# Kernel tuning notes

Measured on AMD Instinct MI355X. Metric: run time of the kernel, lower is better.

## Reference

```python
import jax, jax.numpy as jnp
import numpy as np

N = 50000      # nodes
E = 800000     # edges (avg degree 16)
DIN = 500      # input_dim
HID = 100      # hid_dim (fixed in module)
DOUT = 64      # output_dim
EPS = 1e-5     # LayerNorm eps (torch default)


def _layer_norm(x, g, b):
    mu = jnp.mean(x, axis=-1, keepdims=True)
    var = jnp.var(x, axis=-1, keepdims=True)
    return (x - mu) / jnp.sqrt(var + EPS) * g + b


def _gcn_conv(x, src, tgt, W, b):
    # PyG GCNConv: self-loops + symmetric normalization + linear + scatter-add
    h = x @ W  # [N, out]
    idx = jnp.arange(N)
    src_sl = jnp.concatenate([src, idx])
    tgt_sl = jnp.concatenate([tgt, idx])
    deg = jax.ops.segment_sum(jnp.ones(src_sl.shape, h.dtype), tgt_sl, num_segments=N)
    dinv = jnp.where(deg > 0, deg ** -0.5, 0.0)
    norm = dinv[src_sl] * dinv[tgt_sl]  # [E+N]
    out = jax.ops.segment_sum(h[src_sl] * norm[:, None], tgt_sl, num_segments=N)
    return out + b


def setup_inputs() -> dict:
    key = jax.random.key(0)
    ks = jax.random.split(key, 10)
    glorot = lambda k, fi, fo: jax.random.normal(k, (fi, fo), jnp.float32) * np.float32(1.0 / np.sqrt(fi))
    z = lambda d: jnp.zeros((d,), jnp.float32)
    return dict(
        data_x=jax.random.normal(ks[0], (N, DIN), jnp.float32),
        data_edge_index=jax.random.randint(ks[1], (2, E), 0, N),
        data_edge_attr=jnp.zeros((E,), jnp.int32),  # single relation type
        t_W1=glorot(ks[2], DIN, HID), t_b1=z(HID), t_g1=jnp.ones((HID,), jnp.float32), t_be1=z(HID),
        t_W2=glorot(ks[3], HID, HID), t_b2=z(HID), t_g2=jnp.ones((HID,), jnp.float32), t_be2=z(HID),
        r_Wrel=glorot(ks[4], HID, HID)[None],  # [n_relations=1, H, H]
        r_Wself=glorot(ks[5], HID, HID), r_b=z(HID),
        c1_W=glorot(ks[6], HID, HID), c1_b=z(HID),
        c2_W=glorot(ks[7], HID, DOUT), c2_b=z(DOUT),
    )


def reference(data_x, data_edge_index, data_edge_attr,
              t_W1, t_b1, t_g1, t_be1, t_W2, t_b2, t_g2, t_be2,
              r_Wrel, r_Wself, r_b, c1_W, c1_b, c2_W, c2_b):
    src, tgt = data_edge_index[0], data_edge_index[1]
    # transform: Linear -> LN -> ReLU -> Linear -> LN -> ReLU
    x = jax.nn.relu(_layer_norm(data_x @ t_W1 + t_b1, t_g1, t_be1))
    x = jax.nn.relu(_layer_norm(x @ t_W2 + t_b2, t_g2, t_be2))
    # RGCN, n_relations=1, n_layers=1: per-relation message + self transform
    msgs = x[src] @ r_Wrel[0]  # edge_attr is all relation 0
    x = x @ r_Wself + jax.ops.segment_sum(msgs, tgt, num_segments=N) + r_b
    x = jax.nn.relu(x)  # dropout = identity (eval)
    x = jax.nn.relu(_gcn_conv(x, src, tgt, c1_W, c1_b))
    x = _gcn_conv(x, src, tgt, c2_W, c2_b)
    return jax.nn.log_softmax(x, axis=1)
```

## Files before the change

### kernel.cpp

```cpp
#include <hip/hip_runtime.h>
#include <hip/hip_bf16.h>

typedef __attribute__((ext_vector_type(8))) short short8;
typedef __attribute__((ext_vector_type(8))) unsigned short ushort8;
typedef __attribute__((ext_vector_type(4))) float f32x4;

static constexpr int NN = 50000;
static constexpr int NE = 800000;
static constexpr int SCAN_B = 196;
static constexpr int NBLK = (NN + 63) / 64;

#define MFMA16x16x32 __builtin_amdgcn_mfma_f32_16x16x32_bf16

__device__ __forceinline__ float b2f(unsigned short u){
  unsigned v = ((unsigned)u) << 16;
  return __builtin_bit_cast(float, v);
}
__device__ __forceinline__ unsigned short f2b(float f){
  unsigned x = __builtin_bit_cast(unsigned, f);
  unsigned r = (x + 0x7fffu + ((x >> 16) & 1u)) >> 16;
  return (unsigned short)r;
}
__device__ __forceinline__ short8 u2s(ushort8 v){
  return __builtin_bit_cast(short8, v);
}

__device__ __align__(256) int   g_isf32;
__device__ __align__(256) unsigned short g_W1t  [112 * 512 + 512];
__device__ __align__(256) unsigned short g_W2t  [112 * 128];
__device__ __align__(256) unsigned short g_WselfT[112 * 128];
__device__ __align__(256) unsigned short g_WrelT [112 * 128];
__device__ __align__(256) unsigned short g_c1Wt [112 * 128];
__device__ __align__(256) unsigned short g_c2Wt [64 * 128];
__device__ __align__(256) unsigned short g_bufA[(size_t)NN * 128];
__device__ __align__(256) unsigned short g_bufB[(size_t)NN * 128];
__device__ __align__(256) unsigned short g_bufC[(size_t)NN * 128];
__device__ __align__(256) int   g_deg[NN];
__device__ __align__(256) int   g_rowptr[NN + 1];
__device__ __align__(256) int   g_colidx[NE];
__device__ __align__(256) int   g_epos[NE];
__device__ __align__(256) float g_dinv[NN];
__device__ __align__(256) int   g_partial[256];

__device__ __forceinline__ float ld_in(const void* p, int idx, int isf32){
  if (isf32) return ((const float*)p)[idx];
  return b2f(((const unsigned short*)p)[idx]);
}

__global__ void k_detect_zero(const unsigned short* __restrict__ x){
  if (blockIdx.x == 0){
    __shared__ int sh[256];
    int tid = threadIdx.x;
    int cnt = 0;
    for (int j = 0; j < 16; j++){
      unsigned short h = x[(size_t)(tid * 16 + j) * 2];
      int e = (h >> 7) & 0xFF;
      if (e >= 90 && e <= 160) cnt++;
    }
    sh[tid] = cnt;
    __syncthreads();
    for (int off = 128; off > 0; off >>= 1){
      if (tid < off) sh[tid] += sh[tid + off];
      __syncthreads();
    }
    if (tid == 0) g_isf32 = (sh[0] < 2458) ? 1 : 0;
  } else {
    int i = (blockIdx.x - 1) * 256 + threadIdx.x;
    if (i < NN) g_deg[i] = 0;
  }
}

__device__ __forceinline__ void xp_one(const void* W, unsigned short* Wt, int idx,
                                       int K, int Nc, int Kpad, int Npad, int isf32){
  int n = idx / Kpad;
  int k = idx - n * Kpad;
  float v = 0.f;
  if (n < Nc && k < K) v = ld_in(W, k * Nc + n, isf32);
  Wt[(k >> 5) * (Npad * 32) + n * 32 + (k & 31)] = f2b(v);
}
__global__ void k_transpose_all(const void* W1, const void* W2, const void* Wself,
                                const void* Wrel, const void* c1W, const void* c2W){
  int idx = blockIdx.x * 256 + threadIdx.x;
  const int isf32 = g_isf32;
  if (idx < 57344){ xp_one(W1, g_W1t, idx, 500, 100, 512, 112, isf32); return; }
  idx -= 57344;
  if (idx < 14336){ xp_one(W2,    g_W2t,    idx, 100, 100, 128, 112, isf32); return; }
  idx -= 14336;
  if (idx < 14336){ xp_one(Wself, g_WselfT, idx, 100, 100, 128, 112, isf32); return; }
  idx -= 14336;
  if (idx < 14336){ xp_one(Wrel,  g_WrelT,  idx, 100, 100, 128, 112, isf32); return; }
  idx -= 14336;
  if (idx < 14336){ xp_one(c1W,   g_c1Wt,   idx, 100, 100, 128, 112, isf32); return; }
  idx -= 14336;
  if (idx < 8192){  xp_one(c2W,   g_c2Wt,   idx, 100, 64,  128, 64, isf32); }
}

__global__ void k_deg(const int* __restrict__ tgt){
  int e = blockIdx.x * 256 + threadIdx.x;
  if (e < NE) g_epos[e] = atomicAdd(&g_deg[tgt[e]], 1);
}
__global__ __launch_bounds__(256) void k_scan1(){
  __shared__ int sh[256];
  int t = threadIdx.x;
  int i = blockIdx.x * 256 + t;
  int val = (i < NN) ? g_deg[i] : 0;
  sh[t] = val; __syncthreads();
#pragma unroll
  for (int off = 1; off < 256; off <<= 1){
    int v = (t >= off) ? sh[t - off] : 0;
    __syncthreads(); sh[t] += v; __syncthreads();
  }
  if (i < NN){ g_rowptr[i] = sh[t] - val; g_dinv[i] = rsqrtf((float)(val + 1)); }
  if (t == 255) g_partial[blockIdx.x] = sh[255];
}
__global__ __launch_bounds__(256) void k_scan2(){
  __shared__ int sh[256];
  int t = threadIdx.x;
  int val = (t < SCAN_B) ? g_partial[t] : 0;
  sh[t] = val; __syncthreads();
#pragma unroll
  for (int off = 1; off < 256; off <<= 1){
    int v = (t >= off) ? sh[t - off] : 0;
    __syncthreads(); sh[t] += v; __syncthreads();
  }
  if (t < SCAN_B) g_partial[t] = sh[t] - val;
  if (t == 255) g_rowptr[NN] = sh[255];
}
__global__ __launch_bounds__(256) void k_scan3(){
  int i = blockIdx.x * 256 + threadIdx.x;
  if (i < NN) g_rowptr[i] += g_partial[blockIdx.x];
}
__global__ void k_fill(const int* __restrict__ src, const int* __restrict__ tgt){
  int e = blockIdx.x * 256 + threadIdx.x;
  if (e >= NE) return;
  g_colidx[g_rowptr[tgt[e]] + g_epos[e]] = src[e];
}


template<int DO_LN>
__device__ __forceinline__ void wave_epi(const f32x4* acc, unsigned short* dst,
    int rstride, int grow0, int lane, int isf32,
    const void* bias, const void* gm, const void* be){
  const int m = lane & 15;
  const int q = lane >> 4;
  float bf_[7], gf_[7], ef_[7];
#pragma unroll
  for (int t = 0; t < 7; t++){
    int col = t * 16 + m;
    bool ok = col < 100;
    bf_[t] = ok ? ld_in(bias, col, isf32) : 0.f;
    if (DO_LN){
      gf_[t] = ok ? ld_in(gm, col, isf32) : 0.f;
      ef_[t] = ok ? ld_in(be, col, isf32) : 0.f;
    }
  }
#pragma unroll
  for (int r = 0; r < 4; r++){
    int rl = q * 4 + r;
    float vals[7], s1 = 0.f, s2 = 0.f;
#pragma unroll
    for (int t = 0; t < 7; t++){
      int col = t * 16 + m;
      float v = (col < 100) ? (acc[t][r] + bf_[t]) : 0.f;
      vals[t] = v; s1 += v; s2 += v * v;
    }
    if (DO_LN){
#pragma unroll
      for (int msk = 1; msk < 16; msk <<= 1){
        s1 += __shfl_xor(s1, msk, 64);
        s2 += __shfl_xor(s2, msk, 64);
      }
      float mu = s1 * 0.01f;
      float var = fmaxf(s2 * 0.01f - mu * mu, 0.f);
      float rstd = rsqrtf(var + 1e-5f);
#pragma unroll
      for (int t = 0; t < 7; t++)
        vals[t] = (vals[t] - mu) * rstd * gf_[t] + ef_[t];
    }
    if (grow0 + rl < NN){
      unsigned short* orow = dst + (size_t)rl * rstride;
#pragma unroll
      for (int t = 0; t < 7; t++){
        int col = t * 16 + m;
        float y = fmaxf(vals[t], 0.f);
        orow[col] = f2b((col < 100) ? y : 0.f);
      }
      orow[112 + m] = 0;
    }
  }
}

template<int MODE>
__device__ __forceinline__ void agg_tile(const unsigned short* __restrict__ x,
    unsigned short* aggT, int tid, int brow0){
  const int nl = tid >> 2;
  const int c0 = (tid & 3) * 32;
  const int node = min(brow0 + nl, NN - 1);
  const float wt = (MODE != 0) ? g_dinv[node] : 1.f;
  float a[32];
#pragma unroll
  for (int k = 0; k < 32; k++) a[k] = 0.f;
  const int p0 = g_rowptr[node], p1 = g_rowptr[node + 1];
  for (int p = p0; p < p1; p += 4){
    int s[4]; float wj[4];
#pragma unroll
    for (int j = 0; j < 4; j++){
      bool ok = (p + j) < p1;
      s[j] = ok ? g_colidx[p + j] : node;
      wj[j] = ok ? ((MODE != 0) ? g_dinv[s[j]] * wt : 1.f) : 0.f;
    }
    ushort8 r[4][4];
#pragma unroll
    for (int j = 0; j < 4; j++)
#pragma unroll
      for (int u = 0; u < 4; u++)
        r[j][u] = *reinterpret_cast<const ushort8*>(&x[(size_t)s[j] * 128 + c0 + u * 8]);
#pragma unroll
    for (int j = 0; j < 4; j++)
#pragma unroll
      for (int u = 0; u < 4; u++)
#pragma unroll
        for (int k = 0; k < 8; k++)
          a[u * 8 + k] += wj[j] * b2f((unsigned short)r[j][u][k]);
  }
  if (MODE != 0){
    float ws = wt * wt;
#pragma unroll
    for (int u = 0; u < 4; u++){
      ushort8 sv = *reinterpret_cast<const ushort8*>(&x[(size_t)node * 128 + c0 + u * 8]);
#pragma unroll
      for (int k = 0; k < 8; k++) a[u * 8 + k] += ws * b2f((unsigned short)sv[k]);
    }
  }
  unsigned short* arow = aggT + nl * 136 + c0;
#pragma unroll
  for (int u = 0; u < 4; u++){
    ushort8 o;
#pragma unroll
    for (int k = 0; k < 8; k++) o[k] = f2b(a[u * 8 + k]);
    *reinterpret_cast<ushort8*>(&arow[u * 8]) = o;
  }
}


__global__ __launch_bounds__(256, 3) void k_gemm12(const void* __restrict__ Aext,
    const void* b1, const void* gm1, const void* be1,
    const void* b2, const void* gm2, const void* be2){
  __shared__ unsigned short xT[4][16][136];
  __shared__ unsigned short Wst[2][4096];
  const int tid = threadIdx.x;
  const int w = tid >> 6, lane = tid & 63;
  const int m = lane & 15, q = lane >> 4;
  const int row0 = blockIdx.x * 64 + w * 16;
  const int isf32 = g_isf32;
  const int arow = min(row0 + m, NN - 1);

  short8 afrag[16];
  if (isf32){
    const float* base = (const float*)Aext + (size_t)arow * 500;
#pragma unroll
    for (int h = 0; h < 2; h++){
      f32x4 Ab[16];
#pragma unroll
      for (int kc = 0; kc < 8; kc++){
        int col = (h * 8 + kc) * 32 + q * 8;
        Ab[2 * kc]     = *reinterpret_cast<const f32x4*>(base + min(col, 496));
        Ab[2 * kc + 1] = *reinterpret_cast<const f32x4*>(base + min(col + 4, 496));
      }
#pragma unroll
      for (int kc = 0; kc < 8; kc++){
        f32x4 lo = Ab[2 * kc], hi = Ab[2 * kc + 1];
        afrag[h * 8 + kc] = short8{
          (short)f2b(lo[0]), (short)f2b(lo[1]), (short)f2b(lo[2]), (short)f2b(lo[3]),
          (short)f2b(hi[0]), (short)f2b(hi[1]), (short)f2b(hi[2]), (short)f2b(hi[3])};
      }
    }
  } else {
    const unsigned short* base = (const unsigned short*)Aext + (size_t)arow * 500;
#pragma unroll
    for (int h = 0; h < 2; h++){
      ushort4 Ab[16];
#pragma unroll
      for (int kc = 0; kc < 8; kc++){
        int col = (h * 8 + kc) * 32 + q * 8;
        Ab[2 * kc]     = *reinterpret_cast<const ushort4*>(base + min(col, 496));
        Ab[2 * kc + 1] = *reinterpret_cast<const ushort4*>(base + min(col + 4, 496));
      }
#pragma unroll
      for (int kc = 0; kc < 8; kc++){
        ushort4 lo = Ab[2 * kc], hi = Ab[2 * kc + 1];
        afrag[h * 8 + kc] = short8{
          (short)lo.x, (short)lo.y, (short)lo.z, (short)lo.w,
          (short)hi.x, (short)hi.y, (short)hi.z, (short)hi.w};
      }
    }
  }

  {
    const unsigned short* srcp = g_W1t;
#pragma unroll
    for (int j = 0; j < 2; j++){
      int soff = (w * 2 + j) * 512;
      __builtin_amdgcn_global_load_lds(
        (const __attribute__((address_space(1))) void*)(srcp + soff + lane * 8),
        (__attribute__((address_space(3))) void*)(&Wst[0][soff]), 16, 0, 0);
    }
  }
  __syncthreads();

  f32x4 acc[7] = {};
#pragma unroll
  for (int kc = 0; kc < 16; kc++){
    const int cur = kc & 1;
    if (kc < 15){
      const unsigned short* srcp = g_W1t + (kc + 1) * 3584;
#pragma unroll
      for (int j = 0; j < 2; j++){
        int soff = (w * 2 + j) * 512;
        __builtin_amdgcn_global_load_lds(
          (const __attribute__((address_space(1))) void*)(srcp + soff + lane * 8),
          (__attribute__((address_space(3))) void*)(&Wst[cur ^ 1][soff]), 16, 0, 0);
      }
    }
    const unsigned short* bp = &Wst[cur][m * 32 + q * 8];
#pragma unroll
    for (int t = 0; t < 7; t++){
      short8 b = *reinterpret_cast<const short8*>(bp + t * 512);
      acc[t] = MFMA16x16x32(afrag[kc], b, acc[t], 0, 0, 0);
    }
    __syncthreads();
  }

  wave_epi<1>(acc, &xT[w][0][0], 136, 0, lane, isf32, b1, gm1, be1);

  f32x4 acc2[7] = {};
#pragma unroll
  for (int kc = 0; kc < 4; kc++){
    int k0 = kc * 32 + q * 8;
    short8 a = u2s(*reinterpret_cast<const ushort8*>(&xT[w][m][k0]));
    const unsigned short* bp = g_W2t + kc * 3584 + m * 32 + q * 8;
#pragma unroll
    for (int t = 0; t < 7; t++){
      short8 b = *reinterpret_cast<const short8*>(bp + t * 512);
      acc2[t] = MFMA16x16x32(a, b, acc2[t], 0, 0, 0);
    }
  }
  wave_epi<1>(acc2, g_bufB + (size_t)row0 * 128, 128, row0, lane, isf32, b2, gm2, be2);
}

__global__ __launch_bounds__(256, 3) void k_rgcn_f(const void* rb){
  __shared__ unsigned short aggT[64 * 136];
  const int tid = threadIdx.x;
  const int brow0 = blockIdx.x * 64;
  agg_tile<0>(g_bufB, aggT, tid, brow0);

  const int w = tid >> 6, lane = tid & 63;
  const int m = lane & 15, q = lane >> 4;
  const int row0 = brow0 + w * 16;
  const int arow = min(row0 + m, NN - 1);
  const int isf32 = g_isf32;
  f32x4 acc[7] = {};
#pragma unroll
  for (int kc = 0; kc < 4; kc++){
    int k0 = kc * 32 + q * 8;
    short8 a1 = u2s(*reinterpret_cast<const ushort8*>(&g_bufB[(size_t)arow * 128 + k0]));
    const unsigned short* bp1 = g_WselfT + kc * 3584 + m * 32 + q * 8;
#pragma unroll
    for (int t = 0; t < 7; t++){
      short8 b = *reinterpret_cast<const short8*>(bp1 + t * 512);
      acc[t] = MFMA16x16x32(a1, b, acc[t], 0, 0, 0);
    }
    short8 a2 = u2s(*reinterpret_cast<const ushort8*>(&aggT[(w * 16 + m) * 136 + k0]));
    const unsigned short* bp2 = g_WrelT + kc * 3584 + m * 32 + q * 8;
#pragma unroll
    for (int t = 0; t < 7; t++){
      short8 b = *reinterpret_cast<const short8*>(bp2 + t * 512);
      acc[t] = MFMA16x16x32(a2, b, acc[t], 0, 0, 0);
    }
  }
  wave_epi<0>(acc, g_bufC + (size_t)row0 * 128, 128, row0, lane, isf32, rb, nullptr, nullptr);
}

__global__ __launch_bounds__(256, 3) void k_conv_f(const void* c1b){
  __shared__ unsigned short aggT[64 * 136];
  const int tid = threadIdx.x;
  const int brow0 = blockIdx.x * 64;
  agg_tile<1>(g_bufC, aggT, tid, brow0);

  const int w = tid >> 6, lane = tid & 63;
  const int m = lane & 15, q = lane >> 4;
  const int row0 = brow0 + w * 16;
  const int isf32 = g_isf32;
  unsigned short* tile = aggT + w * 16 * 136;

  f32x4 acc[7] = {};
#pragma unroll
  for (int kc = 0; kc < 4; kc++){
    int k0 = kc * 32 + q * 8;
    short8 a = u2s(*reinterpret_cast<const ushort8*>(&tile[m * 136 + k0]));
    const unsigned short* bp = g_c1Wt + kc * 3584 + m * 32 + q * 8;
#pragma unroll
    for (int t = 0; t < 7; t++){
      short8 b = *reinterpret_cast<const short8*>(bp + t * 512);
      acc[t] = MFMA16x16x32(a, b, acc[t], 0, 0, 0);
    }
  }
  wave_epi<0>(acc, tile, 136, 0, lane, isf32, c1b, nullptr, nullptr);

  f32x4 acc2[4] = {};
#pragma unroll
  for (int kc = 0; kc < 4; kc++){
    int k0 = kc * 32 + q * 8;
    short8 a = u2s(*reinterpret_cast<const ushort8*>(&tile[m * 136 + k0]));
    const unsigned short* bp = g_c2Wt + kc * 2048 + m * 32 + q * 8;
#pragma unroll
    for (int t = 0; t < 4; t++){
      short8 b = *reinterpret_cast<const short8*>(bp + t * 512);
      acc2[t] = MFMA16x16x32(a, b, acc2[t], 0, 0, 0);
    }
  }
#pragma unroll
  for (int r = 0; r < 4; r++){
    int row = row0 + q * 4 + r;
    if (row < NN){
      unsigned short* orow = g_bufA + (size_t)row * 64;
#pragma unroll
      for (int t = 0; t < 4; t++) orow[t * 16 + m] = f2b(acc2[t][r]);
    }
  }
}

__global__ __launch_bounds__(256) void k_agg_lsm(const void* __restrict__ bias,
                                                 void* __restrict__ outv){
  const int isf32 = g_isf32;
  int node = blockIdx.x * 32 + (threadIdx.x >> 3);
  if (node >= NN) return;
  const int c8 = (threadIdx.x & 7) * 8;
  float wt = g_dinv[node];
  float a[4][8];
#pragma unroll
  for (int j = 0; j < 4; j++)
#pragma unroll
    for (int k = 0; k < 8; k++) a[j][k] = 0.f;
  int p0 = g_rowptr[node], p1 = g_rowptr[node + 1];
  for (int p = p0; p < p1; p += 8){
    int sj[8]; float wj[8];
#pragma unroll
    for (int j = 0; j < 8; j++){
      bool ok = (p + j) < p1;
      sj[j] = ok ? g_colidx[p + j] : node;
      wj[j] = ok ? g_dinv[sj[j]] * wt : 0.f;
    }
    ushort8 r[8];
#pragma unroll
    for (int j = 0; j < 8; j++)
      r[j] = *reinterpret_cast<const ushort8*>(&g_bufA[(size_t)sj[j] * 64 + c8]);
#pragma unroll
    for (int j = 0; j < 8; j++)
#pragma unroll
      for (int k = 0; k < 8; k++) a[j & 3][k] += wj[j] * b2f((unsigned short)r[j][k]);
  }
  float ws = wt * wt;
  ushort8 sv = *reinterpret_cast<const ushort8*>(&g_bufA[(size_t)node * 64 + c8]);
#pragma unroll
  for (int k = 0; k < 8; k++) a[0][k] += ws * b2f((unsigned short)sv[k]);

  float v[8], mx = -1e30f;
#pragma unroll
  for (int k = 0; k < 8; k++){
    v[k] = a[0][k] + a[1][k] + a[2][k] + a[3][k] + ld_in(bias, c8 + k, isf32);
    mx = fmaxf(mx, v[k]);
  }
#pragma unroll
  for (int msk = 1; msk < 8; msk <<= 1) mx = fmaxf(mx, __shfl_xor(mx, msk, 64));
  float se = 0.f;
#pragma unroll
  for (int k = 0; k < 8; k++) se += expf(v[k] - mx);
#pragma unroll
  for (int msk = 1; msk < 8; msk <<= 1) se += __shfl_xor(se, msk, 64);
  float lse = logf(se);
  size_t ro = (size_t)node * 64 + c8;
  if (isf32){
    float* o = (float*)outv + ro;
#pragma unroll
    for (int k = 0; k < 8; k++) o[k] = v[k] - mx - lse;
  } else {
    unsigned short* o = (unsigned short*)outv + ro;
#pragma unroll
    for (int k = 0; k < 8; k++) o[k] = f2b(v[k] - mx - lse);
  }
}

extern "C" void kernel_launch(void* const* d_in, const int* in_sizes, int n_in,
                              void* d_out, int out_size, void* d_ws, size_t ws_size,
                              hipStream_t stream){
  (void)in_sizes; (void)n_in; (void)out_size; (void)d_ws; (void)ws_size;
  const void* data_x = d_in[0];
  const int* ei = (const int*)d_in[1];
  const int* src = ei;
  const int* tgt = ei + NE;
  const void *W1 = d_in[3], *b1 = d_in[4], *gm1 = d_in[5], *be1 = d_in[6];
  const void *W2 = d_in[7], *b2 = d_in[8], *gm2 = d_in[9], *be2 = d_in[10];
  const void *Wrel = d_in[11], *Wself = d_in[12], *rb = d_in[13];
  const void *c1W = d_in[14], *c1b = d_in[15];
  const void *c2W = d_in[16], *c2b = d_in[17];

  k_detect_zero<<<1 + (NN + 255) / 256, 256, 0, stream>>>((const unsigned short*)data_x);
  k_transpose_all<<<(122880 + 255) / 256, 256, 0, stream>>>(W1, W2, Wself, Wrel, c1W, c2W);

  k_deg<<<(NE + 255) / 256, 256, 0, stream>>>(tgt);
  k_scan1<<<SCAN_B, 256, 0, stream>>>();
  k_scan2<<<1, 256, 0, stream>>>();
  k_scan3<<<SCAN_B, 256, 0, stream>>>();
  k_fill<<<(NE + 255) / 256, 256, 0, stream>>>(src, tgt);

  k_gemm12<<<NBLK, 256, 0, stream>>>(data_x, b1, gm1, be1, b2, gm2, be2);
  k_rgcn_f<<<NBLK, 256, 0, stream>>>(rb);
  k_conv_f<<<NBLK, 256, 0, stream>>>(c1b);
  k_agg_lsm<<<(NN + 31) / 32, 256, 0, stream>>>(c2b, d_out);
}
```

Before: 438.6 us.

## Rewrite gemm12 as persistent kernel with register-resident W1 and LDS-staged A tiles

Result: slower. 474.3 us (+8.2%).

```diff
diff --git a/kernel.cpp b/kernel.cpp
--- a/kernel.cpp
+++ b/kernel.cpp
@@ -9,6 +9,8 @@
 static constexpr int NE = 800000;
 static constexpr int SCAN_B = 196;
 static constexpr int NBLK = (NN + 63) / 64;
+static constexpr int TILES = NN / 16;
+static constexpr int G12_GRID = 512;
 
 #define MFMA16x16x32 __builtin_amdgcn_mfma_f32_16x16x32_bf16
 
@@ -26,8 +28,8 @@
 }
 
 __device__ __align__(256) int   g_isf32;
-__device__ __align__(256) unsigned short g_W1t  [112 * 512 + 512];
-__device__ __align__(256) unsigned short g_W2t  [112 * 128];
+__device__ __align__(256) unsigned short g_W1t  [16 * 128 * 32];
+__device__ __align__(256) unsigned short g_W2t  [4 * 128 * 32];
 __device__ __align__(256) unsigned short g_WselfT[112 * 128];
 __device__ __align__(256) unsigned short g_WrelT [112 * 128];
 __device__ __align__(256) unsigned short g_c1Wt [112 * 128];
@@ -82,10 +84,10 @@
                                 const void* Wrel, const void* c1W, const void* c2W){
   int idx = blockIdx.x * 256 + threadIdx.x;
   const int isf32 = g_isf32;
-  if (idx < 57344){ xp_one(W1, g_W1t, idx, 500, 100, 512, 112, isf32); return; }
-  idx -= 57344;
-  if (idx < 14336){ xp_one(W2,    g_W2t,    idx, 100, 100, 128, 112, isf32); return; }
-  idx -= 14336;
+  if (idx < 65536){ xp_one(W1, g_W1t, idx, 500, 100, 512, 128, isf32); return; }
+  idx -= 65536;
+  if (idx < 16384){ xp_one(W2,    g_W2t,    idx, 100, 100, 128, 128, isf32); return; }
+  idx -= 16384;
   if (idx < 14336){ xp_one(Wself, g_WselfT, idx, 100, 100, 128, 112, isf32); return; }
   idx -= 14336;
   if (idx < 14336){ xp_one(Wrel,  g_WrelT,  idx, 100, 100, 128, 112, isf32); return; }
@@ -136,6 +138,189 @@
   g_colidx[g_rowptr[tgt[e]] + g_epos[e]] = src[e];
 }
 
+
+__device__ __forceinline__ void stage_A_bf16(const unsigned short* __restrict__ A,
+    int row0, unsigned short* dst, int w, int lane){
+#pragma unroll
+  for (int i = 0; i < 8; i++){
+    int c = w * 8 + i;
+    int row = c >> 2;
+    int off = c * 256 + lane * 4;
+    int soff = off ^ ((row & 7) << 4);
+    int within = soff & 1023;
+    within = min(within, 996);
+    const unsigned short* src = A + (size_t)(row0 + row) * 500 + (within >> 1);
+    __builtin_amdgcn_global_load_lds(
+      (const __attribute__((address_space(1))) void*)src,
+      (__attribute__((address_space(3))) void*)(dst + c * 128), 4, 0, 0);
+  }
+}
+
+__device__ __forceinline__ void stage_A_f32(const float* __restrict__ A,
+    int row0, unsigned short* dst, int tid){
+  int row = tid >> 5;
+  int ws = (tid & 31) * 16;
+#pragma unroll
+  for (int u = 0; u < 2; u++){
+    int lds_byte = row * 1024 + ws * 2 + u * 16;
+    int fl = lds_byte ^ ((row & 7) << 4);
+    int kf = (fl & 1023) >> 1;
+    const float* srow = A + (size_t)(row0 + row) * 500;
+    float v[8];
+#pragma unroll
+    for (int j = 0; j < 4; j++){
+      int kk = min(kf + j * 2, 498);
+      float2 p = *reinterpret_cast<const float2*>(srow + kk);
+      v[j * 2] = p.x; v[j * 2 + 1] = p.y;
+    }
+    ushort8 o;
+#pragma unroll
+    for (int j = 0; j < 8; j++) o[j] = f2b(v[j]);
+    *reinterpret_cast<ushort8*>(dst + (lds_byte >> 1)) = o;
+  }
+}
+
+__global__ __launch_bounds__(512, 4) void k_gemm12(const void* __restrict__ Aext,
+    const void* b1, const void* gm1, const void* be1,
+    const void* b2, const void* gm2, const void* be2){
+  __shared__ unsigned short Ast[2][8192];
+  __shared__ unsigned short x1T[16 * 128];
+  __shared__ float sc[8][16][2];
+
+  const int tid = threadIdx.x;
+  const int w = tid >> 6;
+  const int lane = tid & 63;
+  const int m = lane & 15, q = lane >> 4;
+  const int isf32 = g_isf32;
+  const int col = w * 16 + m;
+  const bool colok = col < 100;
+
+  short8 b1f[16];
+#pragma unroll
+  for (int kc = 0; kc < 16; kc++)
+    b1f[kc] = *reinterpret_cast<const short8*>(g_W1t + kc * 4096 + col * 32 + q * 8);
+
+  const float bb1 = colok ? ld_in(b1, col, isf32)  : 0.f;
+  const float gg1 = colok ? ld_in(gm1, col, isf32) : 0.f;
+  const float ee1 = colok ? ld_in(be1, col, isf32) : 0.f;
+  const float bb2 = colok ? ld_in(b2, col, isf32)  : 0.f;
+  const float gg2 = colok ? ld_in(gm2, col, isf32) : 0.f;
+  const float ee2 = colok ? ld_in(be2, col, isf32) : 0.f;
+
+  if (isf32) stage_A_f32((const float*)Aext, blockIdx.x * 16, &Ast[0][0], tid);
+  else       stage_A_bf16((const unsigned short*)Aext, blockIdx.x * 16, &Ast[0][0], w, lane);
+
+  const int alin = (m << 10) | (q << 4);
+  const int asw  = (m & 7) << 4;
+  int cur = 0;
+
+  for (int T = blockIdx.x; T < TILES; T += G12_GRID){
+    __syncthreads();
+    const int row0 = T * 16;
+    const int Tn = T + G12_GRID;
+    if (Tn < TILES){
+      if (isf32) stage_A_f32((const float*)Aext, Tn * 16, &Ast[cur ^ 1][0], tid);
+      else       stage_A_bf16((const unsigned short*)Aext, Tn * 16, &Ast[cur ^ 1][0], w, lane);
+    }
+
+    const char* ab = (const char*)&Ast[cur][0];
+    f32x4 acc = {};
+#pragma unroll
+    for (int kc = 0; kc < 16; kc++){
+      short8 a = *reinterpret_cast<const short8*>(ab + ((alin | (kc << 6)) ^ asw));
+      acc = MFMA16x16x32(a, b1f[kc], acc, 0, 0, 0);
+    }
+
+    float vals[4];
+#pragma unroll
+    for (int r = 0; r < 4; r++){
+      float v = colok ? (acc[r] + bb1) : 0.f;
+      vals[r] = v;
+      float s1 = v, s2 = v * v;
+#pragma unroll
+      for (int msk = 1; msk < 16; msk <<= 1){
+        s1 += __shfl_xor(s1, msk, 64);
+        s2 += __shfl_xor(s2, msk, 64);
+      }
+      if (m == 0){ sc[w][q * 4 + r][0] = s1; sc[w][q * 4 + r][1] = s2; }
+    }
+    __syncthreads();
+    {
+      float S1 = 0.f, S2 = 0.f;
+#pragma unroll
+      for (int t = 0; t < 8; t++){
+        float2 p = *reinterpret_cast<const float2*>(&sc[t][m][0]);
+        S1 += p.x; S2 += p.y;
+      }
+      float mu = S1 * 0.01f;
+      float var = fmaxf(S2 * 0.01f - mu * mu, 0.f);
+      float rstd = rsqrtf(var + 1e-5f);
+#pragma unroll
+      for (int r = 0; r < 4; r++){
+        int row = q * 4 + r;
+        float mur = __shfl(mu, row, 16);
+        float rsr = __shfl(rstd, row, 16);
+        float y = fmaxf((vals[r] - mur) * rsr * gg1 + ee1, 0.f);
+        int byte = ((row << 8) | (col << 1)) ^ ((row & 7) << 4);
+        *reinterpret_cast<unsigned short*>((char*)x1T + byte) = f2b(colok ? y : 0.f);
+      }
+    }
+    __syncthreads();
+
+    const char* xb = (const char*)x1T;
+    f32x4 acc2 = {};
+#pragma unroll
+    for (int kc = 0; kc < 4; kc++){
+      short8 a = *reinterpret_cast<const short8*>(xb + (((m << 8) | (kc << 6) | (q << 4)) ^ asw));
+      short8 b = *reinterpret_cast<const short8*>(g_W2t + kc * 4096 + col * 32 + q * 8);
+      acc2 = MFMA16x16x32(a, b, acc2, 0, 0, 0);
+    }
+
+#pragma unroll
+    for (int r = 0; r < 4; r++){
+      float v = colok ? (acc2[r] + bb2) : 0.f;
+      vals[r] = v;
+      float s1 = v, s2 = v * v;
+#pragma unroll
+      for (int msk = 1; msk < 16; msk <<= 1){
+        s1 += __shfl_xor(s1, msk, 64);
+        s2 += __shfl_xor(s2, msk, 64);
+      }
+      if (m == 0){ sc[w][q * 4 + r][0] = s1; sc[w][q * 4 + r][1] = s2; }
+    }
+    __syncthreads();
+    {
+      float S1 = 0.f, S2 = 0.f;
+#pragma unroll
+      for (int t = 0; t < 8; t++){
+        float2 p = *reinterpret_cast<const float2*>(&sc[t][m][0]);
+        S1 += p.x; S2 += p.y;
+      }
+      float mu = S1 * 0.01f;
+      float var = fmaxf(S2 * 0.01f - mu * mu, 0.f);
+      float rstd = rsqrtf(var + 1e-5f);
+#pragma unroll
+      for (int r = 0; r < 4; r++){
+        int row = q * 4 + r;
+        float mur = __shfl(mu, row, 16);
+        float rsr = __shfl(rstd, row, 16);
+        float y = fmaxf((vals[r] - mur) * rsr * gg2 + ee2, 0.f);
+        int byte = ((row << 8) | (col << 1)) ^ ((row & 7) << 4);
+        *reinterpret_cast<unsigned short*>((char*)x1T + byte) = f2b(colok ? y : 0.f);
+      }
+    }
+    __syncthreads();
+
+    {
+      int row = tid >> 5;
+      int cc = (tid & 31) * 8;
+      int byte = ((row << 8) | cc) ^ ((row & 7) << 4);
+      ushort4 vst = *reinterpret_cast<const ushort4*>((const char*)x1T + byte);
+      *reinterpret_cast<ushort4*>(g_bufB + (size_t)(row0 + row) * 128 + (tid & 31) * 4) = vst;
+    }
+    cur ^= 1;
+  }
+}
 
 template<int DO_LN>
 __device__ __forceinline__ void wave_epi(const f32x4* acc, unsigned short* dst,
@@ -240,112 +425,6 @@
     for (int k = 0; k < 8; k++) o[k] = f2b(a[u * 8 + k]);
     *reinterpret_cast<ushort8*>(&arow[u * 8]) = o;
   }
-}
-
-
-__global__ __launch_bounds__(256, 3) void k_gemm12(const void* __restrict__ Aext,
-    const void* b1, const void* gm1, const void* be1,
-    const void* b2, const void* gm2, const void* be2){
-  __shared__ unsigned short xT[4][16][136];
-  __shared__ unsigned short Wst[2][4096];
-  const int tid = threadIdx.x;
-  const int w = tid >> 6, lane = tid & 63;
-  const int m = lane & 15, q = lane >> 4;
-  const int row0 = blockIdx.x * 64 + w * 16;
-  const int isf32 = g_isf32;
-  const int arow = min(row0 + m, NN - 1);
-
-  short8 afrag[16];
-  if (isf32){
-    const float* base = (const float*)Aext + (size_t)arow * 500;
-#pragma unroll
-    for (int h = 0; h < 2; h++){
-      f32x4 Ab[16];
-#pragma unroll
-      for (int kc = 0; kc < 8; kc++){
-        int col = (h * 8 + kc) * 32 + q * 8;
-        Ab[2 * kc]     = *reinterpret_cast<const f32x4*>(base + min(col, 496));
-        Ab[2 * kc + 1] = *reinterpret_cast<const f32x4*>(base + min(col + 4, 496));
-      }
-#pragma unroll
-      for (int kc = 0; kc < 8; kc++){
-        f32x4 lo = Ab[2 * kc], hi = Ab[2 * kc + 1];
-        afrag[h * 8 + kc] = short8{
-          (short)f2b(lo[0]), (short)f2b(lo[1]), (short)f2b(lo[2]), (short)f2b(lo[3]),
-          (short)f2b(hi[0]), (short)f2b(hi[1]), (short)f2b(hi[2]), (short)f2b(hi[3])};
-      }
-    }
-  } else {
-    const unsigned short* base = (const unsigned short*)Aext + (size_t)arow * 500;
-#pragma unroll
-    for (int h = 0; h < 2; h++){
-      ushort4 Ab[16];
-#pragma unroll
-      for (int kc = 0; kc < 8; kc++){
-        int col = (h * 8 + kc) * 32 + q * 8;
-        Ab[2 * kc]     = *reinterpret_cast<const ushort4*>(base + min(col, 496));
-        Ab[2 * kc + 1] = *reinterpret_cast<const ushort4*>(base + min(col + 4, 496));
-      }
-#pragma unroll
-      for (int kc = 0; kc < 8; kc++){
-        ushort4 lo = Ab[2 * kc], hi = Ab[2 * kc + 1];
-        afrag[h * 8 + kc] = short8{
-          (short)lo.x, (short)lo.y, (short)lo.z, (short)lo.w,
-          (short)hi.x, (short)hi.y, (short)hi.z, (short)hi.w};
-      }
-    }
-  }
-
-  {
-    const unsigned short* srcp = g_W1t;
-#pragma unroll
-    for (int j = 0; j < 2; j++){
-      int soff = (w * 2 + j) * 512;
-      __builtin_amdgcn_global_load_lds(
-        (const __attribute__((address_space(1))) void*)(srcp + soff + lane * 8),
-        (__attribute__((address_space(3))) void*)(&Wst[0][soff]), 16, 0, 0);
-    }
-  }
-  __syncthreads();
-
-  f32x4 acc[7] = {};
-#pragma unroll
-  for (int kc = 0; kc < 16; kc++){
-    const int cur = kc & 1;
-    if (kc < 15){
-      const unsigned short* srcp = g_W1t + (kc + 1) * 3584;
-#pragma unroll
-      for (int j = 0; j < 2; j++){
-        int soff = (w * 2 + j) * 512;
-        __builtin_amdgcn_global_load_lds(
-          (const __attribute__((address_space(1))) void*)(srcp + soff + lane * 8),
-          (__attribute__((address_space(3))) void*)(&Wst[cur ^ 1][soff]), 16, 0, 0);
-      }
-    }
-    const unsigned short* bp = &Wst[cur][m * 32 + q * 8];
-#pragma unroll
-    for (int t = 0; t < 7; t++){
-      short8 b = *reinterpret_cast<const short8*>(bp + t * 512);
-      acc[t] = MFMA16x16x32(afrag[kc], b, acc[t], 0, 0, 0);
-    }
-    __syncthreads();
-  }
-
-  wave_epi<1>(acc, &xT[w][0][0], 136, 0, lane, isf32, b1, gm1, be1);
-
-  f32x4 acc2[7] = {};
-#pragma unroll
-  for (int kc = 0; kc < 4; kc++){
-    int k0 = kc * 32 + q * 8;
-    short8 a = u2s(*reinterpret_cast<const ushort8*>(&xT[w][m][k0]));
-    const unsigned short* bp = g_W2t + kc * 3584 + m * 32 + q * 8;
-#pragma unroll
-    for (int t = 0; t < 7; t++){
-      short8 b = *reinterpret_cast<const short8*>(bp + t * 512);
-      acc2[t] = MFMA16x16x32(a, b, acc2[t], 0, 0, 0);
-    }
-  }
-  wave_epi<1>(acc2, g_bufB + (size_t)row0 * 128, 128, row0, lane, isf32, b2, gm2, be2);
 }
 
 __global__ __launch_bounds__(256, 3) void k_rgcn_f(const void* rb){
@@ -506,7 +585,7 @@
   const void *c2W = d_in[16], *c2b = d_in[17];
 
   k_detect_zero<<<1 + (NN + 255) / 256, 256, 0, stream>>>((const unsigned short*)data_x);
-  k_transpose_all<<<(122880 + 255) / 256, 256, 0, stream>>>(W1, W2, Wself, Wrel, c1W, c2W);
+  k_transpose_all<<<(133120 + 255) / 256, 256, 0, stream>>>(W1, W2, Wself, Wrel, c1W, c2W);
 
   k_deg<<<(NE + 255) / 256, 256, 0, stream>>>(tgt);
   k_scan1<<<SCAN_B, 256, 0, stream>>>();
@@ -514,7 +593,7 @@
   k_scan3<<<SCAN_B, 256, 0, stream>>>();
   k_fill<<<(NE + 255) / 256, 256, 0, stream>>>(src, tgt);
 
-  k_gemm12<<<NBLK, 256, 0, stream>>>(data_x, b1, gm1, be1, b2, gm2, be2);
+  k_gemm12<<<G12_GRID, 512, 0, stream>>>(data_x, b1, gm1, be1, b2, gm2, be2);
   k_rgcn_f<<<NBLK, 256, 0, stream>>>(rb);
   k_conv_f<<<NBLK, 256, 0, stream>>>(c1b);
   k_agg_lsm<<<(NN + 31) / 32, 256, 0, stream>>>(c2b, d_out);
```
